# Performance work log

Measured on AMD Instinct MI355X. Metric: run time of the kernel, lower is better.

## Reference

```python
import jax, jax.numpy as jnp
import numpy as np

N_NODES = 100000
N_EDGES = 1600000
IN_FEATS = 64
HIDDEN = 128


def setup_inputs() -> dict:
    key = jax.random.key(0)
    k1, k2, k3, k4 = jax.random.split(key, 4)
    X = jax.random.normal(k1, (N_NODES, IN_FEATS), dtype=jnp.float32)
    edge_index = jax.random.randint(k2, (2, N_EDGES), 0, N_NODES, dtype=jnp.int64)
    W1 = jax.random.normal(k3, (IN_FEATS, HIDDEN), dtype=jnp.float32) * (1.0 / np.sqrt(IN_FEATS))
    b1 = jnp.zeros((HIDDEN,), dtype=jnp.float32)
    W2 = jax.random.normal(k4, (HIDDEN, 1), dtype=jnp.float32) * (1.0 / np.sqrt(HIDDEN))
    b2 = jnp.zeros((1,), dtype=jnp.float32)
    return {"X": X, "edge_index": edge_index, "W1": W1, "b1": b1, "W2": W2, "b2": b2}


def _gcn_conv(X, src, dst, norm, W, b, n_nodes):
    # GCNConv: out = D^{-1/2} (A + I) D^{-1/2} (X @ W) + b
    h = X @ W                       # [N, out_feats]
    msg = h[src] * norm[:, None]    # gather + per-edge scale
    out = jax.ops.segment_sum(msg, dst, num_segments=n_nodes)
    return out + b


def _norm_and_loops(edge_index, n_nodes):
    # add self loops and compute symmetric normalization coefficients
    loop = jnp.arange(n_nodes, dtype=edge_index.dtype)
    src = jnp.concatenate([edge_index[0], loop])
    dst = jnp.concatenate([edge_index[1], loop])
    deg = jax.ops.segment_sum(jnp.ones_like(dst, dtype=jnp.float32), dst,
                              num_segments=n_nodes)  # deg >= 1 (self loop)
    dinv = jax.lax.rsqrt(deg)
    norm = dinv[src] * dinv[dst]    # [E + N]
    return src, dst, norm


def reference(X, edge_index, W1, b1, W2, b2):
    n_nodes = X.shape[0]
    src, dst, norm = _norm_and_loops(edge_index, n_nodes)
    h = jax.nn.relu(_gcn_conv(X, src, dst, norm, W1, b1, n_nodes))
    # dropout omitted (stochastic; identity for deterministic reference)
    out = _gcn_conv(h, src, dst, norm, W2, b2, n_nodes)
    return out
```

## Files before the change

### kernel.cpp

```cpp
#include <hip/hip_runtime.h>
#include <hip/hip_fp16.h>


#define INF 64
#define HID 128
#define BKBITS 9
#define BKSZ 512
#define TILE_E 8192
#define TOW 257

using half8 = __attribute__((ext_vector_type(8))) _Float16;
using f32x4 = __attribute__((ext_vector_type(4))) float;

__global__ __launch_bounds__(1024) void k_histbin(const int* __restrict__ srcA,
                                                  const int* __restrict__ dstA,
                                                  int* __restrict__ tileOff,
                                                  unsigned* __restrict__ binned,
                                                  int nE, int nt,
                                                  const float* __restrict__ W1,
                                                  _Float16* __restrict__ W1t) {
    int tid = threadIdx.x;
    int bx = blockIdx.x;
    if (bx == nt) {
        for (int i = tid; i < HID * INF; i += 1024) {
            int nCol = i >> 6;
            int k = i & 63;
            W1t[i] = (_Float16)W1[k * HID + nCol];
        }
        return;
    }
    __shared__ int hist[256];
    __shared__ int curs[256];
    if (tid < 256) hist[tid] = 0;
    __syncthreads();
    int base = bx * TILE_E;
    int d[8], s[8];
#pragma unroll
    for (int k = 0; k < 8; ++k) {
        int e = base + k * 1024 + tid;
        if (e < nE) {
            d[k] = dstA[e];
            s[k] = srcA[e];
            atomicAdd(&hist[((unsigned)d[k]) >> BKBITS], 1);
        } else {
            d[k] = -1;
        }
    }
    __syncthreads();
    int own = (tid < 256) ? hist[tid] : 0;
    for (int off = 1; off < 256; off <<= 1) {
        int u = (tid < 256 && tid >= off) ? hist[tid - off] : 0;
        __syncthreads();
        if (tid < 256) hist[tid] += u;
        __syncthreads();
    }
    if (tid < 256) {
        int ex = hist[tid] - own;
        curs[tid] = ex;
        tileOff[bx * TOW + tid] = ex;
        if (tid == 255) tileOff[bx * TOW + 256] = hist[255];
    }
    __syncthreads();
#pragma unroll
    for (int k = 0; k < 8; ++k) {
        if (d[k] >= 0) {
            int bk = ((unsigned)d[k]) >> BKBITS;
            int off = atomicAdd(&curs[bk], 1);
            binned[base + off] = ((unsigned)(d[k] & (BKSZ - 1)) << 17) | (unsigned)s[k];
        }
    }
}

__global__ __launch_bounds__(1024) void k_csr(const unsigned* __restrict__ binned,
                                              const int* __restrict__ tileOff,
                                              int* __restrict__ rowPtr,
                                              float* __restrict__ dinv,
                                              int* __restrict__ eSrc,
                                              const float4* __restrict__ X4,
                                              uint4* __restrict__ Xs4,
                                              int n, int nt, int nbk) {
    __shared__ int segS[256], segL[256];
    __shared__ int hist[512];
    __shared__ int curs[512];
    __shared__ float ddv[512];
    __shared__ int bBaseS;
    int tid = threadIdx.x;
    int b = blockIdx.x;
    if (tid == 0) bBaseS = 0;
    if (tid < 512) hist[tid] = 0;
    __syncthreads();
    if (tid < nt) {
        int o0 = tileOff[tid * TOW + b];
        int o1 = tileOff[tid * TOW + b + 1];
        segS[tid] = tid * TILE_E + o0;
        segL[tid] = o1 - o0;
        atomicAdd(&bBaseS, o0);
    }
    __syncthreads();
    int w = tid >> 6, lane = tid & 63;
    for (int t = w; t < nt; t += 16)
        for (int l = lane; l < segL[t]; l += 64)
            atomicAdd(&hist[binned[segS[t] + l] >> 17], 1);
    __syncthreads();
    int own = (tid < 512) ? hist[tid] : 0;
    for (int off = 1; off < 512; off <<= 1) {
        int u = (tid < 512 && tid >= off) ? hist[tid - off] : 0;
        __syncthreads();
        if (tid < 512) hist[tid] += u;
        __syncthreads();
    }
    int bBase = bBaseS;
    if (tid < 512) {
        int pos0 = bBase + hist[tid] - own;
        curs[tid] = pos0;
        float dD = rsqrtf((float)(own + 1));
        ddv[tid] = dD;
        int node = (b << BKBITS) + tid;
        if (node < n) {
            rowPtr[node] = pos0;
            dinv[node] = dD;
        }
        if (b == nbk - 1 && tid == 511) rowPtr[n] = bBase + hist[511];
    }
    __syncthreads();
    for (int t = w; t < nt; t += 16)
        for (int l = lane; l < segL[t]; l += 64) {
            unsigned v = binned[segS[t] + l];
            int pos = atomicAdd(&curs[v >> 17], 1);
            eSrc[pos] = (int)(v & 0x1FFFFu);
        }
    int nbase = b << BKBITS;
#pragma unroll
    for (int k2 = 0; k2 < 4; ++k2) {
        int t2 = k2 * 1024 + tid;
        int nl = t2 >> 3;
        int r2 = t2 & 7;
        int node2 = nbase + nl;
        if (node2 < n) {
            float dD2 = ddv[nl];
            float4 a = X4[(size_t)node2 * 16 + r2 * 2];
            float4 bb = X4[(size_t)node2 * 16 + r2 * 2 + 1];
            __half2 h0 = __float22half2_rn(make_float2(dD2 * a.x, dD2 * a.y));
            __half2 h1 = __float22half2_rn(make_float2(dD2 * a.z, dD2 * a.w));
            __half2 h2 = __float22half2_rn(make_float2(dD2 * bb.x, dD2 * bb.y));
            __half2 h3 = __float22half2_rn(make_float2(dD2 * bb.z, dD2 * bb.w));
            uint4 o;
            o.x = *(unsigned*)&h0; o.y = *(unsigned*)&h1;
            o.z = *(unsigned*)&h2; o.w = *(unsigned*)&h3;
            Xs4[(size_t)node2 * 8 + r2] = o;
        }
    }
}

__device__ inline void acc8_add(const uint4& v, float* acc) {
    const __half2* hp = (const __half2*)&v;
#pragma unroll
    for (int i = 0; i < 4; ++i) {
        float2 f = __half22float2(hp[i]);
        acc[2 * i]     += f.x;
        acc[2 * i + 1] += f.y;
    }
}

__global__ __launch_bounds__(256) void k_agg_mlp(const uint4* __restrict__ Xs4,
                                                 const int* __restrict__ rowPtr,
                                                 const int* __restrict__ eSrc,
                                                 const float* __restrict__ dinv,
                                                 const uint4* __restrict__ W1t4,
                                                 const float* __restrict__ b1,
                                                 const float* __restrict__ W2,
                                                 float* __restrict__ svs, int n) {
    __shared__ __align__(16) unsigned short W1s[HID * INF];
    __shared__ __align__(16) unsigned short aggS[32 * INF];
    __shared__ float b1s[HID];
    __shared__ float W2s[HID];
    int tid = threadIdx.x;

    for (int i = tid; i < HID * 8; i += 256) {
        int c = i >> 3, cb = i & 7;
        uint4 v = W1t4[i];
        int off = c * 128 + ((cb * 16) ^ ((c & 7) << 4));
        *(uint4*)((char*)W1s + off) = v;
    }
    if (tid < HID) {
        b1s[tid] = b1[tid];
        W2s[tid] = W2[tid];
    }

    int node0 = blockIdx.x * 32;
    int w = tid >> 3;
    int r = tid & 7;
    int node = node0 + w;
    if (node < n) {
        int beg = rowPtr[node];
        int end = rowPtr[node + 1];
        float dD = dinv[node];
        float acc[8];
        {
            uint4 v = Xs4[(size_t)node * 8 + r];
            const __half2* hp = (const __half2*)&v;
#pragma unroll
            for (int i = 0; i < 4; ++i) {
                float2 f = __half22float2(hp[i]);
                acc[2 * i] = f.x;
                acc[2 * i + 1] = f.y;
            }
        }
        int j = beg;
        int aEnd = min(end, (beg + 3) & ~3);
        for (; j < aEnd; ++j) {
            uint4 v = Xs4[(size_t)eSrc[j] * 8 + r];
            acc8_add(v, acc);
        }
        for (; j + 7 < end; j += 8) {
            int4 sa = *(const int4*)(eSrc + j);
            int4 sb = *(const int4*)(eSrc + j + 4);
            uint4 v0 = Xs4[(size_t)sa.x * 8 + r];
            uint4 v1 = Xs4[(size_t)sa.y * 8 + r];
            uint4 v2 = Xs4[(size_t)sa.z * 8 + r];
            uint4 v3 = Xs4[(size_t)sa.w * 8 + r];
            uint4 v4 = Xs4[(size_t)sb.x * 8 + r];
            uint4 v5 = Xs4[(size_t)sb.y * 8 + r];
            uint4 v6 = Xs4[(size_t)sb.z * 8 + r];
            uint4 v7 = Xs4[(size_t)sb.w * 8 + r];
            acc8_add(v0, acc); acc8_add(v1, acc); acc8_add(v2, acc); acc8_add(v3, acc);
            acc8_add(v4, acc); acc8_add(v5, acc); acc8_add(v6, acc); acc8_add(v7, acc);
        }
        if (j + 3 < end) {
            int4 s4 = *(const int4*)(eSrc + j);
            uint4 v0 = Xs4[(size_t)s4.x * 8 + r];
            uint4 v1 = Xs4[(size_t)s4.y * 8 + r];
            uint4 v2 = Xs4[(size_t)s4.z * 8 + r];
            uint4 v3 = Xs4[(size_t)s4.w * 8 + r];
            acc8_add(v0, acc); acc8_add(v1, acc); acc8_add(v2, acc); acc8_add(v3, acc);
            j += 4;
        }
        for (; j < end; ++j) {
            uint4 v = Xs4[(size_t)eSrc[j] * 8 + r];
            acc8_add(v, acc);
        }
        __half2 h0 = __float22half2_rn(make_float2(dD * acc[0], dD * acc[1]));
        __half2 h1 = __float22half2_rn(make_float2(dD * acc[2], dD * acc[3]));
        __half2 h2 = __float22half2_rn(make_float2(dD * acc[4], dD * acc[5]));
        __half2 h3 = __float22half2_rn(make_float2(dD * acc[6], dD * acc[7]));
        uint4 o;
        o.x = *(unsigned*)&h0; o.y = *(unsigned*)&h1;
        o.z = *(unsigned*)&h2; o.w = *(unsigned*)&h3;
        int off = w * 128 + ((r * 16) ^ ((w & 7) << 4));
        *(uint4*)((char*)aggS + off) = o;
    }
    __syncthreads();

    int wave = tid >> 6;
    if (wave < 2) {
        int l = tid & 63;
        int row16 = l & 15;
        int kg = l >> 4;
        int lrow = wave * 16 + row16;
        int swzA = (lrow & 7) << 4;
        half8 a0 = *(const half8*)((const char*)aggS + lrow * 128 + ((kg * 16) ^ swzA));
        half8 a1 = *(const half8*)((const char*)aggS + lrow * 128 + ((64 + kg * 16) ^ swzA));
        float p0 = 0.0f, p1 = 0.0f, p2 = 0.0f, p3 = 0.0f;
#pragma unroll
        for (int nt = 0; nt < 8; ++nt) {
            int c = nt * 16 + row16;
            int swzB = (c & 7) << 4;
            half8 bf0 = *(const half8*)((const char*)W1s + c * 128 + ((kg * 16) ^ swzB));
            half8 bf1 = *(const half8*)((const char*)W1s + c * 128 + ((64 + kg * 16) ^ swzB));
            f32x4 acc4 = {0.0f, 0.0f, 0.0f, 0.0f};
            acc4 = __builtin_amdgcn_mfma_f32_16x16x32_f16(a0, bf0, acc4, 0, 0, 0);
            acc4 = __builtin_amdgcn_mfma_f32_16x16x32_f16(a1, bf1, acc4, 0, 0, 0);
            float b1v = b1s[c];
            float w2v = W2s[c];
            float h;
            h = fmaxf(acc4[0] + b1v, 0.0f); p0 = fmaf(h, w2v, p0);
            h = fmaxf(acc4[1] + b1v, 0.0f); p1 = fmaf(h, w2v, p1);
            h = fmaxf(acc4[2] + b1v, 0.0f); p2 = fmaf(h, w2v, p2);
            h = fmaxf(acc4[3] + b1v, 0.0f); p3 = fmaf(h, w2v, p3);
        }
#pragma unroll
        for (int off = 1; off < 16; off <<= 1) {
            p0 += __shfl_xor(p0, off, 64);
            p1 += __shfl_xor(p1, off, 64);
            p2 += __shfl_xor(p2, off, 64);
            p3 += __shfl_xor(p3, off, 64);
        }
        if (row16 == 0) {
            int nd = node0 + wave * 16 + kg * 4;
            if (nd + 0 < n) svs[nd + 0] = dinv[nd + 0] * p0;
            if (nd + 1 < n) svs[nd + 1] = dinv[nd + 1] * p1;
            if (nd + 2 < n) svs[nd + 2] = dinv[nd + 2] * p2;
            if (nd + 3 < n) svs[nd + 3] = dinv[nd + 3] * p3;
        }
    }
}

__global__ __launch_bounds__(256) void k_out(const int* __restrict__ rowPtr,
                                             const int* __restrict__ eSrc,
                                             const float* __restrict__ dinv,
                                             const float* __restrict__ svs,
                                             const float* __restrict__ b2,
                                             float* __restrict__ out, int n) {
    int t = blockIdx.x * blockDim.x + threadIdx.x;
    int node = t >> 4;
    int r = t & 15;
    if (node >= n) return;
    int beg = rowPtr[node];
    int end = rowPtr[node + 1];
    float p = 0.0f;
    for (int j = beg + r; j < end; j += 16) p += svs[eSrc[j]];
    p += __shfl_xor(p, 1, 16);
    p += __shfl_xor(p, 2, 16);
    p += __shfl_xor(p, 4, 16);
    p += __shfl_xor(p, 8, 16);
    if (r == 0) {
        float dD = dinv[node];
        out[node] = fmaf(dD, p + svs[node], b2[0]);
    }
}

extern "C" void kernel_launch(void* const* d_in, const int* in_sizes, int n_in,
                              void* d_out, int out_size, void* d_ws, size_t ws_size,
                              hipStream_t stream) {
    const float* X  = (const float*)d_in[0];
    const int*   ei = (const int*)d_in[1];
    const float* W1 = (const float*)d_in[2];
    const float* b1 = (const float*)d_in[3];
    const float* W2 = (const float*)d_in[4];
    const float* b2 = (const float*)d_in[5];

    int N = in_sizes[0] / INF;
    int E = in_sizes[1] / 2;
    const int* srcA = ei;
    const int* dstA = ei + E;

    int nt  = (E + TILE_E - 1) / TILE_E;
    int nbk = (N + BKSZ - 1) >> BKBITS;

    uint4*    Xs4      = (uint4*)d_ws;
    unsigned* binned   = (unsigned*)(Xs4 + (size_t)N * 8);
    int*      eSrc     = (int*)(binned + (size_t)nt * TILE_E);
    _Float16* W1t      = (_Float16*)(eSrc + E);
    int*      tileOff  = (int*)(W1t + HID * INF);
    int*      rowPtr   = tileOff + nt * TOW;
    float*    dinv     = (float*)(rowPtr + N + 1);
    float*    svs      = dinv + N;
    float*    out      = (float*)d_out;

    k_histbin<<<nt + 1, 1024, 0, stream>>>(srcA, dstA, tileOff, binned, E, nt, W1, W1t);
    k_csr<<<nbk, 1024, 0, stream>>>(binned, tileOff, rowPtr, dinv, eSrc,
                                    (const float4*)X, Xs4, N, nt, nbk);
    k_agg_mlp<<<(N + 31) / 32, 256, 0, stream>>>(Xs4, rowPtr, eSrc, dinv,
                                                 (const uint4*)W1t, b1, W2, svs, N);
    k_out<<<(N * 16 + 255) / 256, 256, 0, stream>>>(rowPtr, eSrc, dinv, svs, b2, out, N);
}
```

Before: 93.39 us.

## Split feature aggregation into four column-slice passes and separate MLP kernel

Stores the scaled fp16 features as four column slices of 16 features each, node-major within each slice. Aggregation then runs as four kernel launches, each gathering a 3.2 MB slice so the random neighbour reads stay cache resident. The fused MFMA MLP moves into its own kernel, which reads the aggregated slices from global memory and keeps W1 in registers. This costs extra launches, one extra write and read of the aggregated matrix, and four passes over the CSR index arrays.

```diff
diff --git a/kernel.cpp b/kernel.cpp
--- a/kernel.cpp
+++ b/kernel.cpp
@@ -77,7 +77,7 @@
                                               float* __restrict__ dinv,
                                               int* __restrict__ eSrc,
                                               const float4* __restrict__ X4,
-                                              uint4* __restrict__ Xs4,
+                                              uint4* __restrict__ Xt,
                                               int n, int nt, int nbk) {
     __shared__ int segS[256], segL[256];
     __shared__ int hist[512];
@@ -147,11 +147,20 @@
             uint4 o;
             o.x = *(unsigned*)&h0; o.y = *(unsigned*)&h1;
             o.z = *(unsigned*)&h2; o.w = *(unsigned*)&h3;
-            Xs4[(size_t)node2 * 8 + r2] = o;
-        }
-    }
-}
-
+            Xt[(size_t)(r2 >> 1) * n * 2 + (size_t)node2 * 2 + (r2 & 1)] = o;
+        }
+    }
+}
+
+__device__ inline void acc8_set(const uint4& v, float* acc) {
+    const __half2* hp = (const __half2*)&v;
+#pragma unroll
+    for (int i = 0; i < 4; ++i) {
+        float2 f = __half22float2(hp[i]);
+        acc[2 * i] = f.x;
+        acc[2 * i + 1] = f.y;
+    }
+}
 __device__ inline void acc8_add(const uint4& v, float* acc) {
     const __half2* hp = (const __half2*)&v;
 #pragma unroll
@@ -162,136 +171,118 @@
     }
 }
 
-__global__ __launch_bounds__(256) void k_agg_mlp(const uint4* __restrict__ Xs4,
-                                                 const int* __restrict__ rowPtr,
-                                                 const int* __restrict__ eSrc,
-                                                 const float* __restrict__ dinv,
-                                                 const uint4* __restrict__ W1t4,
-                                                 const float* __restrict__ b1,
-                                                 const float* __restrict__ W2,
-                                                 float* __restrict__ svs, int n) {
-    __shared__ __align__(16) unsigned short W1s[HID * INF];
-    __shared__ __align__(16) unsigned short aggS[32 * INF];
-    __shared__ float b1s[HID];
-    __shared__ float W2s[HID];
-    int tid = threadIdx.x;
-
-    for (int i = tid; i < HID * 8; i += 256) {
-        int c = i >> 3, cb = i & 7;
-        uint4 v = W1t4[i];
-        int off = c * 128 + ((cb * 16) ^ ((c & 7) << 4));
-        *(uint4*)((char*)W1s + off) = v;
-    }
-    if (tid < HID) {
-        b1s[tid] = b1[tid];
-        W2s[tid] = W2[tid];
-    }
-
-    int node0 = blockIdx.x * 32;
-    int w = tid >> 3;
-    int r = tid & 7;
-    int node = node0 + w;
-    if (node < n) {
-        int beg = rowPtr[node];
-        int end = rowPtr[node + 1];
-        float dD = dinv[node];
-        float acc[8];
-        {
-            uint4 v = Xs4[(size_t)node * 8 + r];
-            const __half2* hp = (const __half2*)&v;
-#pragma unroll
-            for (int i = 0; i < 4; ++i) {
-                float2 f = __half22float2(hp[i]);
-                acc[2 * i] = f.x;
-                acc[2 * i + 1] = f.y;
-            }
-        }
-        int j = beg;
-        int aEnd = min(end, (beg + 3) & ~3);
-        for (; j < aEnd; ++j) {
-            uint4 v = Xs4[(size_t)eSrc[j] * 8 + r];
-            acc8_add(v, acc);
-        }
-        for (; j + 7 < end; j += 8) {
-            int4 sa = *(const int4*)(eSrc + j);
-            int4 sb = *(const int4*)(eSrc + j + 4);
-            uint4 v0 = Xs4[(size_t)sa.x * 8 + r];
-            uint4 v1 = Xs4[(size_t)sa.y * 8 + r];
-            uint4 v2 = Xs4[(size_t)sa.z * 8 + r];
-            uint4 v3 = Xs4[(size_t)sa.w * 8 + r];
-            uint4 v4 = Xs4[(size_t)sb.x * 8 + r];
-            uint4 v5 = Xs4[(size_t)sb.y * 8 + r];
-            uint4 v6 = Xs4[(size_t)sb.z * 8 + r];
-            uint4 v7 = Xs4[(size_t)sb.w * 8 + r];
-            acc8_add(v0, acc); acc8_add(v1, acc); acc8_add(v2, acc); acc8_add(v3, acc);
-            acc8_add(v4, acc); acc8_add(v5, acc); acc8_add(v6, acc); acc8_add(v7, acc);
-        }
-        if (j + 3 < end) {
-            int4 s4 = *(const int4*)(eSrc + j);
-            uint4 v0 = Xs4[(size_t)s4.x * 8 + r];
-            uint4 v1 = Xs4[(size_t)s4.y * 8 + r];
-            uint4 v2 = Xs4[(size_t)s4.z * 8 + r];
-            uint4 v3 = Xs4[(size_t)s4.w * 8 + r];
-            acc8_add(v0, acc); acc8_add(v1, acc); acc8_add(v2, acc); acc8_add(v3, acc);
-            j += 4;
-        }
-        for (; j < end; ++j) {
-            uint4 v = Xs4[(size_t)eSrc[j] * 8 + r];
-            acc8_add(v, acc);
-        }
-        __half2 h0 = __float22half2_rn(make_float2(dD * acc[0], dD * acc[1]));
-        __half2 h1 = __float22half2_rn(make_float2(dD * acc[2], dD * acc[3]));
-        __half2 h2 = __float22half2_rn(make_float2(dD * acc[4], dD * acc[5]));
-        __half2 h3 = __float22half2_rn(make_float2(dD * acc[6], dD * acc[7]));
-        uint4 o;
-        o.x = *(unsigned*)&h0; o.y = *(unsigned*)&h1;
-        o.z = *(unsigned*)&h2; o.w = *(unsigned*)&h3;
-        int off = w * 128 + ((r * 16) ^ ((w & 7) << 4));
-        *(uint4*)((char*)aggS + off) = o;
-    }
-    __syncthreads();
-
-    int wave = tid >> 6;
-    if (wave < 2) {
-        int l = tid & 63;
-        int row16 = l & 15;
-        int kg = l >> 4;
-        int lrow = wave * 16 + row16;
-        int swzA = (lrow & 7) << 4;
-        half8 a0 = *(const half8*)((const char*)aggS + lrow * 128 + ((kg * 16) ^ swzA));
-        half8 a1 = *(const half8*)((const char*)aggS + lrow * 128 + ((64 + kg * 16) ^ swzA));
-        float p0 = 0.0f, p1 = 0.0f, p2 = 0.0f, p3 = 0.0f;
-#pragma unroll
-        for (int nt = 0; nt < 8; ++nt) {
-            int c = nt * 16 + row16;
-            int swzB = (c & 7) << 4;
-            half8 bf0 = *(const half8*)((const char*)W1s + c * 128 + ((kg * 16) ^ swzB));
-            half8 bf1 = *(const half8*)((const char*)W1s + c * 128 + ((64 + kg * 16) ^ swzB));
-            f32x4 acc4 = {0.0f, 0.0f, 0.0f, 0.0f};
-            acc4 = __builtin_amdgcn_mfma_f32_16x16x32_f16(a0, bf0, acc4, 0, 0, 0);
-            acc4 = __builtin_amdgcn_mfma_f32_16x16x32_f16(a1, bf1, acc4, 0, 0, 0);
-            float b1v = b1s[c];
-            float w2v = W2s[c];
-            float h;
-            h = fmaxf(acc4[0] + b1v, 0.0f); p0 = fmaf(h, w2v, p0);
-            h = fmaxf(acc4[1] + b1v, 0.0f); p1 = fmaf(h, w2v, p1);
-            h = fmaxf(acc4[2] + b1v, 0.0f); p2 = fmaf(h, w2v, p2);
-            h = fmaxf(acc4[3] + b1v, 0.0f); p3 = fmaf(h, w2v, p3);
-        }
-#pragma unroll
-        for (int off = 1; off < 16; off <<= 1) {
-            p0 += __shfl_xor(p0, off, 64);
-            p1 += __shfl_xor(p1, off, 64);
-            p2 += __shfl_xor(p2, off, 64);
-            p3 += __shfl_xor(p3, off, 64);
-        }
-        if (row16 == 0) {
-            int nd = node0 + wave * 16 + kg * 4;
-            if (nd + 0 < n) svs[nd + 0] = dinv[nd + 0] * p0;
-            if (nd + 1 < n) svs[nd + 1] = dinv[nd + 1] * p1;
-            if (nd + 2 < n) svs[nd + 2] = dinv[nd + 2] * p2;
-            if (nd + 3 < n) svs[nd + 3] = dinv[nd + 3] * p3;
-        }
+__global__ __launch_bounds__(256) void k_agg_slice(const uint4* __restrict__ Xt,
+                                                   const int* __restrict__ rowPtr,
+                                                   const int* __restrict__ eSrc,
+                                                   const float* __restrict__ dinv,
+                                                   uint4* __restrict__ aggT,
+                                                   int n, int p) {
+    int gid = blockIdx.x * 256 + threadIdx.x;
+    int node = gid >> 1;
+    int c = gid & 1;
+    if (node >= n) return;
+    const uint4* tab = Xt + (size_t)p * n * 2;
+    int beg = rowPtr[node];
+    int end = rowPtr[node + 1];
+    float dD = dinv[node];
+    float acc[8];
+    acc8_set(tab[(size_t)node * 2 + c], acc);
+    int j = beg;
+    int aEnd = min(end, (beg + 3) & ~3);
+    for (; j < aEnd; ++j) acc8_add(tab[(size_t)eSrc[j] * 2 + c], acc);
+    for (; j + 7 < end; j += 8) {
+        int4 sa = *(const int4*)(eSrc + j);
+        int4 sb = *(const int4*)(eSrc + j + 4);
+        uint4 v0 = tab[(size_t)sa.x * 2 + c];
+        uint4 v1 = tab[(size_t)sa.y * 2 + c];
+        uint4 v2 = tab[(size_t)sa.z * 2 + c];
+        uint4 v3 = tab[(size_t)sa.w * 2 + c];
+        uint4 v4 = tab[(size_t)sb.x * 2 + c];
+        uint4 v5 = tab[(size_t)sb.y * 2 + c];
+        uint4 v6 = tab[(size_t)sb.z * 2 + c];
+        uint4 v7 = tab[(size_t)sb.w * 2 + c];
+        acc8_add(v0, acc); acc8_add(v1, acc); acc8_add(v2, acc); acc8_add(v3, acc);
+        acc8_add(v4, acc); acc8_add(v5, acc); acc8_add(v6, acc); acc8_add(v7, acc);
+    }
+    if (j + 3 < end) {
+        int4 s4 = *(const int4*)(eSrc + j);
+        uint4 v0 = tab[(size_t)s4.x * 2 + c];
+        uint4 v1 = tab[(size_t)s4.y * 2 + c];
+        uint4 v2 = tab[(size_t)s4.z * 2 + c];
+        uint4 v3 = tab[(size_t)s4.w * 2 + c];
+        acc8_add(v0, acc); acc8_add(v1, acc); acc8_add(v2, acc); acc8_add(v3, acc);
+        j += 4;
+    }
+    for (; j < end; ++j) acc8_add(tab[(size_t)eSrc[j] * 2 + c], acc);
+    __half2 h0 = __float22half2_rn(make_float2(dD * acc[0], dD * acc[1]));
+    __half2 h1 = __float22half2_rn(make_float2(dD * acc[2], dD * acc[3]));
+    __half2 h2 = __float22half2_rn(make_float2(dD * acc[4], dD * acc[5]));
+    __half2 h3 = __float22half2_rn(make_float2(dD * acc[6], dD * acc[7]));
+    uint4 o;
+    o.x = *(unsigned*)&h0; o.y = *(unsigned*)&h1;
+    o.z = *(unsigned*)&h2; o.w = *(unsigned*)&h3;
+    aggT[(size_t)p * n * 2 + (size_t)node * 2 + c] = o;
+}
+
+__global__ __launch_bounds__(256) void k_mlp(const uint4* __restrict__ aggT,
+                                             const uint4* __restrict__ W1t4,
+                                             const float* __restrict__ b1,
+                                             const float* __restrict__ W2,
+                                             const float* __restrict__ dinv,
+                                             float* __restrict__ svs,
+                                             int nTiles, int n) {
+    int lane = threadIdx.x & 63;
+    int tile = (blockIdx.x * blockDim.x + threadIdx.x) >> 6;
+    if (tile >= nTiles) return;
+    int m0 = tile * 16;
+    int row = lane & 15;
+    int kg = lane >> 4;
+
+    half8 bf[8][2];
+    float b1v[8], w2v[8];
+#pragma unroll
+    for (int nt = 0; nt < 8; ++nt) {
+        int col = nt * 16 + row;
+#pragma unroll
+        for (int ks = 0; ks < 2; ++ks) {
+            uint4 u = W1t4[col * 8 + ks * 4 + kg];
+            bf[nt][ks] = __builtin_bit_cast(half8, u);
+        }
+        b1v[nt] = b1[col];
+        w2v[nt] = W2[col];
+    }
+
+    int node = m0 + row;
+    uint4 ua0 = aggT[(size_t)(kg >> 1) * n * 2 + (size_t)node * 2 + (kg & 1)];
+    uint4 ua1 = aggT[(size_t)(2 + (kg >> 1)) * n * 2 + (size_t)node * 2 + (kg & 1)];
+    half8 a0 = __builtin_bit_cast(half8, ua0);
+    half8 a1 = __builtin_bit_cast(half8, ua1);
+
+    float p0 = 0.0f, p1 = 0.0f, p2 = 0.0f, p3 = 0.0f;
+#pragma unroll
+    for (int nt = 0; nt < 8; ++nt) {
+        f32x4 acc = {0.0f, 0.0f, 0.0f, 0.0f};
+        acc = __builtin_amdgcn_mfma_f32_16x16x32_f16(a0, bf[nt][0], acc, 0, 0, 0);
+        acc = __builtin_amdgcn_mfma_f32_16x16x32_f16(a1, bf[nt][1], acc, 0, 0, 0);
+        float h;
+        h = fmaxf(acc[0] + b1v[nt], 0.0f); p0 = fmaf(h, w2v[nt], p0);
+        h = fmaxf(acc[1] + b1v[nt], 0.0f); p1 = fmaf(h, w2v[nt], p1);
+        h = fmaxf(acc[2] + b1v[nt], 0.0f); p2 = fmaf(h, w2v[nt], p2);
+        h = fmaxf(acc[3] + b1v[nt], 0.0f); p3 = fmaf(h, w2v[nt], p3);
+    }
+#pragma unroll
+    for (int off = 1; off < 16; off <<= 1) {
+        p0 += __shfl_xor(p0, off, 64);
+        p1 += __shfl_xor(p1, off, 64);
+        p2 += __shfl_xor(p2, off, 64);
+        p3 += __shfl_xor(p3, off, 64);
+    }
+    if (row == 0) {
+        int nd = m0 + kg * 4;
+        if (nd + 0 < n) svs[nd + 0] = dinv[nd + 0] * p0;
+        if (nd + 1 < n) svs[nd + 1] = dinv[nd + 1] * p1;
+        if (nd + 2 < n) svs[nd + 2] = dinv[nd + 2] * p2;
+        if (nd + 3 < n) svs[nd + 3] = dinv[nd + 3] * p3;
     }
 }
 
@@ -337,8 +328,9 @@
     int nt  = (E + TILE_E - 1) / TILE_E;
     int nbk = (N + BKSZ - 1) >> BKBITS;
 
-    uint4*    Xs4      = (uint4*)d_ws;
-    unsigned* binned   = (unsigned*)(Xs4 + (size_t)N * 8);
+    uint4*    Xt       = (uint4*)d_ws;
+    uint4*    aggT     = Xt + (size_t)N * 8;
+    unsigned* binned   = (unsigned*)(aggT + (size_t)N * 8);
     int*      eSrc     = (int*)(binned + (size_t)nt * TILE_E);
     _Float16* W1t      = (_Float16*)(eSrc + E);
     int*      tileOff  = (int*)(W1t + HID * INF);
@@ -347,10 +339,15 @@
     float*    svs      = dinv + N;
     float*    out      = (float*)d_out;
 
+    int nTiles = (N + 15) / 16;
+
     k_histbin<<<nt + 1, 1024, 0, stream>>>(srcA, dstA, tileOff, binned, E, nt, W1, W1t);
     k_csr<<<nbk, 1024, 0, stream>>>(binned, tileOff, rowPtr, dinv, eSrc,
-                                    (const float4*)X, Xs4, N, nt, nbk);
-    k_agg_mlp<<<(N + 31) / 32, 256, 0, stream>>>(Xs4, rowPtr, eSrc, dinv,
-                                                 (const uint4*)W1t, b1, W2, svs, N);
+                                    (const float4*)X, Xt, N, nt, nbk);
+    for (int p = 0; p < 4; ++p)
+        k_agg_slice<<<(N * 2 + 255) / 256, 256, 0, stream>>>(Xt, rowPtr, eSrc,
+                                                             dinv, aggT, N, p);
+    k_mlp<<<(nTiles * 64 + 255) / 256, 256, 0, stream>>>(aggT, (const uint4*)W1t,
+                                                         b1, W2, dinv, svs, nTiles, N);
     k_out<<<(N * 16 + 255) / 256, 256, 0, stream>>>(rowPtr, eSrc, dinv, svs, b2, out, N);
 }
```

After: 135.6 us. 1.45x slower.

## Shrink CSR buckets, cache bucket records in LDS, use wave-shuffle scans

Applied to the files above, without the earlier changes.

Bucket size drops from 512 to 256 nodes and tiles from 8192 to 6144 edges. This roughly doubles the number of k_csr blocks (512 threads each) and adds more histbin tiles, giving more parallelism in the CSR build. k_csr now stages its binned records in a shared-memory buffer (up to 5120 entries) during the histogram pass, so the scatter pass reads from LDS instead of global memory, falling back to global on overflow. The LDS barrier-heavy prefix scans are replaced with wave shuffle scans plus a per-wave sum. Risks are larger tileOff tables, more segments per block, and extra LDS use that may lower occupancy.

```diff
diff --git a/kernel.cpp b/kernel.cpp
--- a/kernel.cpp
+++ b/kernel.cpp
@@ -4,10 +4,12 @@
 
 #define INF 64
 #define HID 128
-#define BKBITS 9
-#define BKSZ 512
-#define TILE_E 8192
-#define TOW 257
+#define BKBITS 8
+#define BKSZ 256
+#define TILE_E 6144
+#define EPT 6
+#define SEGMAX 384
+#define CAP 5120
 
 using half8 = __attribute__((ext_vector_type(8))) _Float16;
 using f32x4 = __attribute__((ext_vector_type(4))) float;
@@ -16,7 +18,7 @@
                                                   const int* __restrict__ dstA,
                                                   int* __restrict__ tileOff,
                                                   unsigned* __restrict__ binned,
-                                                  int nE, int nt,
+                                                  int nE, int nt, int nbk,
                                                   const float* __restrict__ W1,
                                                   _Float16* __restrict__ W1t) {
     int tid = threadIdx.x;
@@ -29,14 +31,15 @@
         }
         return;
     }
-    __shared__ int hist[256];
-    __shared__ int curs[256];
-    if (tid < 256) hist[tid] = 0;
+    __shared__ int hist[512];
+    __shared__ int curs[512];
+    __shared__ int wsum[8];
+    if (tid < 512) hist[tid] = 0;
     __syncthreads();
     int base = bx * TILE_E;
-    int d[8], s[8];
-#pragma unroll
-    for (int k = 0; k < 8; ++k) {
+    int d[EPT], s[EPT];
+#pragma unroll
+    for (int k = 0; k < EPT; ++k) {
         int e = base + k * 1024 + tid;
         if (e < nE) {
             d[k] = dstA[e];
@@ -47,22 +50,28 @@
         }
     }
     __syncthreads();
-    int own = (tid < 256) ? hist[tid] : 0;
-    for (int off = 1; off < 256; off <<= 1) {
-        int u = (tid < 256 && tid >= off) ? hist[tid - off] : 0;
-        __syncthreads();
-        if (tid < 256) hist[tid] += u;
-        __syncthreads();
-    }
-    if (tid < 256) {
-        int ex = hist[tid] - own;
+    int lane = tid & 63, wv = tid >> 6;
+    int v = 0, own = 0;
+    if (tid < 512) {
+        v = hist[tid];
+        own = v;
+#pragma unroll
+        for (int off = 1; off < 64; off <<= 1) {
+            int u = __shfl_up(v, off, 64);
+            if (lane >= off) v += u;
+        }
+        if (lane == 63) wsum[wv] = v;
+    }
+    __syncthreads();
+    if (tid < 512) {
+        for (int g = 0; g < wv; ++g) v += wsum[g];
+        int ex = v - own;
         curs[tid] = ex;
-        tileOff[bx * TOW + tid] = ex;
-        if (tid == 255) tileOff[bx * TOW + 256] = hist[255];
-    }
-    __syncthreads();
-#pragma unroll
-    for (int k = 0; k < 8; ++k) {
+        if (tid <= nbk) tileOff[bx * (nbk + 1) + tid] = ex;
+    }
+    __syncthreads();
+#pragma unroll
+    for (int k = 0; k < EPT; ++k) {
         if (d[k] >= 0) {
             int bk = ((unsigned)d[k]) >> BKBITS;
             int off = atomicAdd(&curs[bk], 1);
@@ -71,68 +80,92 @@
     }
 }
 
-__global__ __launch_bounds__(1024) void k_csr(const unsigned* __restrict__ binned,
-                                              const int* __restrict__ tileOff,
-                                              int* __restrict__ rowPtr,
-                                              float* __restrict__ dinv,
-                                              int* __restrict__ eSrc,
-                                              const float4* __restrict__ X4,
-                                              uint4* __restrict__ Xs4,
-                                              int n, int nt, int nbk) {
-    __shared__ int segS[256], segL[256];
-    __shared__ int hist[512];
-    __shared__ int curs[512];
-    __shared__ float ddv[512];
+__global__ __launch_bounds__(512) void k_csr(const unsigned* __restrict__ binned,
+                                             const int* __restrict__ tileOff,
+                                             int* __restrict__ rowPtr,
+                                             float* __restrict__ dinv,
+                                             int* __restrict__ eSrc,
+                                             const float4* __restrict__ X4,
+                                             uint4* __restrict__ Xs4,
+                                             int n, int nt, int nbk) {
+    __shared__ int segG[SEGMAX], segL[SEGMAX], segO[SEGMAX];
+    __shared__ int hist[BKSZ], curs[BKSZ];
+    __shared__ float ddv[BKSZ];
+    __shared__ unsigned ldsRec[CAP];
+    __shared__ int wsum[8];
     __shared__ int bBaseS;
     int tid = threadIdx.x;
     int b = blockIdx.x;
     if (tid == 0) bBaseS = 0;
-    if (tid < 512) hist[tid] = 0;
-    __syncthreads();
-    if (tid < nt) {
-        int o0 = tileOff[tid * TOW + b];
-        int o1 = tileOff[tid * TOW + b + 1];
-        segS[tid] = tid * TILE_E + o0;
-        segL[tid] = o1 - o0;
+    if (tid < BKSZ) hist[tid] = 0;
+    __syncthreads();
+    for (int t = tid; t < nt; t += 512) {
+        int o0 = tileOff[t * (nbk + 1) + b];
+        int o1 = tileOff[t * (nbk + 1) + b + 1];
+        segG[t] = t * TILE_E + o0;
+        segL[t] = o1 - o0;
         atomicAdd(&bBaseS, o0);
     }
     __syncthreads();
-    int w = tid >> 6, lane = tid & 63;
-    for (int t = w; t < nt; t += 16)
-        for (int l = lane; l < segL[t]; l += 64)
-            atomicAdd(&hist[binned[segS[t] + l] >> 17], 1);
-    __syncthreads();
-    int own = (tid < 512) ? hist[tid] : 0;
-    for (int off = 1; off < 512; off <<= 1) {
-        int u = (tid < 512 && tid >= off) ? hist[tid - off] : 0;
-        __syncthreads();
-        if (tid < 512) hist[tid] += u;
-        __syncthreads();
-    }
+    int lane = tid & 63, wv = tid >> 6;
+    int v = (tid < nt) ? segL[tid] : 0;
+    int own = v;
+#pragma unroll
+    for (int off = 1; off < 64; off <<= 1) {
+        int u = __shfl_up(v, off, 64);
+        if (lane >= off) v += u;
+    }
+    if (lane == 63) wsum[wv] = v;
+    __syncthreads();
+    for (int g = 0; g < wv; ++g) v += wsum[g];
+    if (tid < nt) segO[tid] = v - own;
+    __syncthreads();
+    int g16 = tid >> 4, l16 = tid & 15;
+    for (int t = g16; t < nt; t += 32) {
+        int L = segL[t], G = segG[t], O = segO[t];
+        for (int l = l16; l < L; l += 16) {
+            unsigned u = binned[G + l];
+            int idx = O + l;
+            if (idx < CAP) ldsRec[idx] = u;
+            atomicAdd(&hist[u >> 17], 1);
+        }
+    }
+    __syncthreads();
+    int v2 = (tid < BKSZ) ? hist[tid] : 0;
+    int own2 = v2;
+#pragma unroll
+    for (int off = 1; off < 64; off <<= 1) {
+        int u = __shfl_up(v2, off, 64);
+        if (lane >= off) v2 += u;
+    }
+    if (lane == 63) wsum[wv] = v2;
+    __syncthreads();
+    for (int g = 0; g < wv; ++g) v2 += wsum[g];
     int bBase = bBaseS;
-    if (tid < 512) {
-        int pos0 = bBase + hist[tid] - own;
+    if (tid < BKSZ) {
+        int pos0 = bBase + v2 - own2;
         curs[tid] = pos0;
-        float dD = rsqrtf((float)(own + 1));
+        float dD = rsqrtf((float)(own2 + 1));
         ddv[tid] = dD;
         int node = (b << BKBITS) + tid;
         if (node < n) {
             rowPtr[node] = pos0;
             dinv[node] = dD;
         }
-        if (b == nbk - 1 && tid == 511) rowPtr[n] = bBase + hist[511];
-    }
-    __syncthreads();
-    for (int t = w; t < nt; t += 16)
-        for (int l = lane; l < segL[t]; l += 64) {
-            unsigned v = binned[segS[t] + l];
-            int pos = atomicAdd(&curs[v >> 17], 1);
-            eSrc[pos] = (int)(v & 0x1FFFFu);
-        }
+        if (b == nbk - 1 && tid == BKSZ - 1) rowPtr[n] = bBase + v2;
+    }
+    __syncthreads();
+    for (int t = g16; t < nt; t += 32) {
+        int L = segL[t], G = segG[t], O = segO[t];
+        for (int l = l16; l < L; l += 16) {
+            int idx = O + l;
+            unsigned u = (idx < CAP) ? ldsRec[idx] : binned[G + l];
+            int pos = atomicAdd(&curs[u >> 17], 1);
+            eSrc[pos] = (int)(u & 0x1FFFFu);
+        }
+    }
     int nbase = b << BKBITS;
-#pragma unroll
-    for (int k2 = 0; k2 < 4; ++k2) {
-        int t2 = k2 * 1024 + tid;
+    for (int t2 = tid; t2 < BKSZ * 8; t2 += 512) {
         int nl = t2 >> 3;
         int r2 = t2 & 7;
         int node2 = nbase + nl;
@@ -262,8 +295,8 @@
         half8 a1 = *(const half8*)((const char*)aggS + lrow * 128 + ((64 + kg * 16) ^ swzA));
         float p0 = 0.0f, p1 = 0.0f, p2 = 0.0f, p3 = 0.0f;
 #pragma unroll
-        for (int nt = 0; nt < 8; ++nt) {
-            int c = nt * 16 + row16;
+        for (int nt2 = 0; nt2 < 8; ++nt2) {
+            int c = nt2 * 16 + row16;
             int swzB = (c & 7) << 4;
             half8 bf0 = *(const half8*)((const char*)W1s + c * 128 + ((kg * 16) ^ swzB));
             half8 bf1 = *(const half8*)((const char*)W1s + c * 128 + ((64 + kg * 16) ^ swzB));
@@ -342,14 +375,15 @@
     int*      eSrc     = (int*)(binned + (size_t)nt * TILE_E);
     _Float16* W1t      = (_Float16*)(eSrc + E);
     int*      tileOff  = (int*)(W1t + HID * INF);
-    int*      rowPtr   = tileOff + nt * TOW;
+    int*      rowPtr   = tileOff + nt * (nbk + 1);
     float*    dinv     = (float*)(rowPtr + N + 1);
     float*    svs      = dinv + N;
     float*    out      = (float*)d_out;
 
-    k_histbin<<<nt + 1, 1024, 0, stream>>>(srcA, dstA, tileOff, binned, E, nt, W1, W1t);
-    k_csr<<<nbk, 1024, 0, stream>>>(binned, tileOff, rowPtr, dinv, eSrc,
-                                    (const float4*)X, Xs4, N, nt, nbk);
+    k_histbin<<<nt + 1, 1024, 0, stream>>>(srcA, dstA, tileOff, binned, E, nt, nbk,
+                                           W1, W1t);
+    k_csr<<<nbk, 512, 0, stream>>>(binned, tileOff, rowPtr, dinv, eSrc,
+                                   (const float4*)X, Xs4, N, nt, nbk);
     k_agg_mlp<<<(N + 31) / 32, 256, 0, stream>>>(Xs4, rowPtr, eSrc, dinv,
                                                  (const uint4*)W1t, b1, W2, svs, N);
     k_out<<<(N * 16 + 255) / 256, 256, 0, stream>>>(rowPtr, eSrc, dinv, svs, b2, out, N);
```

Result: no change. 94.25 us (+0.9%).
